# Performance work log

Measured on AMD Instinct MI355X. Metric: run time of the kernel, lower is better.

The kernel has to match this reference:

```python
import jax, jax.numpy as jnp
import numpy as np
from jax import lax

D_MODEL = 256
D_INNER = 512   # expand=2
D_STATE = 16
D_CONV = 4
DT_RANK = 16    # ceil(256/16)
HID = 128
NCLS = 4


def setup_inputs() -> dict:
    key = jax.random.key(0)
    ks = jax.random.split(key, 20)
    B, L = 4, 2048
    s = lambda *sh: 1.0 / np.sqrt(np.prod(sh[1:]) if len(sh) > 1 else sh[0])
    inp = {
        'x': jax.random.normal(ks[0], (B, L, 9), jnp.float32),
        'conv1_w': jax.random.normal(ks[1], (HID, 9, 3), jnp.float32) * s(HID, 9, 3),
        'conv1_b': jnp.zeros((HID,), jnp.float32),
        'conv2_w': jax.random.normal(ks[2], (2 * HID, HID, 3), jnp.float32) * s(2 * HID, HID, 3),
        'conv2_b': jnp.zeros((2 * HID,), jnp.float32),
        'in_proj_w': jax.random.normal(ks[3], (2 * D_INNER, D_MODEL), jnp.float32) * s(2 * D_INNER, D_MODEL),
        'dw_conv_w': jax.random.normal(ks[4], (D_INNER, 1, D_CONV), jnp.float32) * 0.5,
        'dw_conv_b': jnp.zeros((D_INNER,), jnp.float32),
        'x_proj_w': jax.random.normal(ks[5], (DT_RANK + 2 * D_STATE, D_INNER), jnp.float32) * s(1, D_INNER),
        'dt_proj_w': jax.random.normal(ks[6], (D_INNER, DT_RANK), jnp.float32) * s(D_INNER, DT_RANK),
        'dt_proj_b': jnp.log(jnp.expm1(jnp.full((D_INNER,), 0.01, jnp.float32))),  # dt init ~0.01
        'A_log': jnp.log(jnp.broadcast_to(jnp.arange(1, D_STATE + 1, dtype=jnp.float32), (D_INNER, D_STATE))).copy(),
        'D_param': jnp.ones((D_INNER,), jnp.float32),
        'out_proj_w': jax.random.normal(ks[7], (D_MODEL, D_INNER), jnp.float32) * s(D_MODEL, D_INNER),
        'fc1_w': jax.random.normal(ks[8], (HID, D_MODEL), jnp.float32) * s(HID, D_MODEL),
        'fc1_b': jnp.zeros((HID,), jnp.float32),
        'fc2_w': jax.random.normal(ks[9], (NCLS, HID), jnp.float32) * s(NCLS, HID),
        'fc2_b': jnp.zeros((NCLS,), jnp.float32),
    }
    return inp


def _conv1d(x, w, b, pad):
    # x: [B,C,L], w: [O,I,K]
    y = lax.conv_general_dilated(x, w, (1,), [pad], dimension_numbers=('NCH', 'OIH', 'NCH'))
    return y + b[None, :, None]


def _selective_scan(u, dt, Bm, Cm, A, D_param):
    # u, dt: [B,L,di]; Bm, Cm: [B,L,ds]; A: [di,ds]
    def step(h, inp):
        dt_t, b_t, c_t, u_t = inp  # [B,di],[B,ds],[B,ds],[B,di]
        dA = jnp.exp(dt_t[:, :, None] * A[None])            # [B,di,ds]
        dBu = (dt_t * u_t)[:, :, None] * b_t[:, None, :]     # [B,di,ds]
        h = dA * h + dBu
        y = jnp.einsum('bds,bs->bd', h, c_t)
        return h, y

    Bsz = u.shape[0]
    h0 = jnp.zeros((Bsz, D_INNER, D_STATE), u.dtype)
    xs = (dt.transpose(1, 0, 2), Bm.transpose(1, 0, 2), Cm.transpose(1, 0, 2), u.transpose(1, 0, 2))
    _, ys = lax.scan(step, h0, xs)
    y = ys.transpose(1, 0, 2)  # [B,L,di]
    return y + u * D_param[None, None, :]


def _forward(x, conv1_w, conv1_b, conv2_w, conv2_b, in_proj_w, dw_conv_w, dw_conv_b,
             x_proj_w, dt_proj_w, dt_proj_b, A_log, D_param, out_proj_w,
             fc1_w, fc1_b, fc2_w, fc2_b):
    # Conv feature stack
    data = x.transpose(0, 2, 1)                       # [B,9,L]
    f = jax.nn.relu(_conv1d(data, conv1_w, conv1_b, (1, 1)))
    f = jax.nn.relu(_conv1d(f, conv2_w, conv2_b, (1, 1)))
    feat = f.transpose(0, 2, 1)                       # [B,L,256]

    # Mamba block
    xz = feat @ in_proj_w.T                           # [B,L,1024]
    x_in, z = jnp.split(xz, 2, axis=-1)               # [B,L,512] each
    xc = x_in.transpose(0, 2, 1)                      # [B,512,L]
    xc = lax.conv_general_dilated(xc, dw_conv_w, (1,), [(D_CONV - 1, 0)],
                                  dimension_numbers=('NCH', 'OIH', 'NCH'),
                                  feature_group_count=D_INNER)
    xc = xc + dw_conv_b[None, :, None]
    u = jax.nn.silu(xc).transpose(0, 2, 1)            # [B,L,512]

    x_dbl = u @ x_proj_w.T                            # [B,L,48]
    dt_lr = x_dbl[..., :DT_RANK]
    Bm = x_dbl[..., DT_RANK:DT_RANK + D_STATE]
    Cm = x_dbl[..., DT_RANK + D_STATE:]
    dt = jax.nn.softplus(dt_lr @ dt_proj_w.T + dt_proj_b)  # [B,L,512]
    A = -jnp.exp(A_log)                               # [512,16]

    y = _selective_scan(u, dt, Bm, Cm, A, D_param)
    y = y * jax.nn.silu(z)
    mamba_out = y @ out_proj_w.T                      # [B,L,256]

    pooled = jnp.max(mamba_out, axis=1)               # [B,256]
    h = jax.nn.relu(pooled @ fc1_w.T + fc1_b)
    return h @ fc2_w.T + fc2_b                        # [B,4]


def reference(x, conv1_w, conv1_b, conv2_w, conv2_b, in_proj_w, dw_conv_w, dw_conv_b,
              x_proj_w, dt_proj_w, dt_proj_b, A_log, D_param, out_proj_w,
              fc1_w, fc1_b, fc2_w, fc2_b):
    return _forward(x, conv1_w, conv1_b, conv2_w, conv2_b, in_proj_w, dw_conv_w, dw_conv_b,
                    x_proj_w, dt_proj_w, dt_proj_b, A_log, D_param, out_proj_w,
                    fc1_w, fc1_b, fc2_w, fc2_b)
```

## Files before the change

### kernel.cpp

```cpp
#include <hip/hip_runtime.h>
#include <cfloat>

#define BB 4
#define LL 2048
#define DSTATE 16
#define CH 32
#define NC 64

typedef unsigned short u16;
typedef __attribute__((ext_vector_type(8))) short bf16x8;
typedef __attribute__((ext_vector_type(4))) float f32x4;

__device__ inline u16 f2b(float v) {
  union { float f; unsigned u; } c; c.f = v;
  unsigned r = c.u + 0x7fffu + ((c.u >> 16) & 1u);
  return (u16)(r >> 16);
}
__device__ inline float b2f(u16 h) {
  union { unsigned u; float f; } c; c.u = ((unsigned)h) << 16;
  return c.f;
}
__device__ inline void atomicMaxF(float* a, float v) {
  if (v >= 0.f) atomicMax((int*)a, __float_as_int(v));
  else atomicMin((unsigned int*)a, __float_as_uint(v));
}

#define GLOAD16(gsrc, ldst) \
  __builtin_amdgcn_global_load_lds( \
      (const __attribute__((address_space(1))) unsigned int*)(gsrc), \
      (__attribute__((address_space(3))) unsigned int*)(ldst), 16, 0, 0)

__global__ __launch_bounds__(256) void k1_conv1A(const float* __restrict__ x,
    const float* __restrict__ w, const float* __restrict__ bias,
    u16* __restrict__ A) {
  int idx = blockIdx.x * 256 + threadIdx.x;
  int i = idx & 127;
  int t = (idx >> 7) & (LL - 1);
  int b = idx >> 18;
  float acc = bias[i];
#pragma unroll
  for (int k = 0; k < 3; ++k) {
    int ts = t + k - 1;
    if (ts < 0 || ts >= LL) continue;
    const float* xr = x + (b * LL + ts) * 9;
    const float* wr = w + i * 27 + k;
#pragma unroll
    for (int c = 0; c < 9; ++c) acc += xr[c] * wr[c * 3];
  }
  float v = fmaxf(acc, 0.f);
  u16 h = f2b(v), l = f2b(v - b2f(h));
#pragma unroll
  for (int tap = 0; tap < 3; ++tap) {
    int rr = t + 1 - tap;
    if (rr < 0 || rr >= LL) continue;
    u16* rp = A + ((size_t)(b * LL + rr)) * 1152 + tap * 128 + i;
    rp[0] = h; rp[384] = l; rp[768] = h;
  }
  if (t == 0) {
    u16* rp = A + ((size_t)(b * LL)) * 1152 + i;
    rp[0] = 0; rp[384] = 0; rp[768] = 0;
  }
  if (t == LL - 1) {
    u16* rp = A + ((size_t)(b * LL + LL - 1)) * 1152 + 256 + i;
    rp[0] = 0; rp[384] = 0; rp[768] = 0;
  }
}

__global__ __launch_bounds__(256) void k_prep(const float* __restrict__ wc2,
    const float* __restrict__ wip, const float* __restrict__ wop,
    u16* __restrict__ dc2, u16* __restrict__ dip, u16* __restrict__ dop,
    float* __restrict__ pooled) {
  int idx = blockIdx.x * 256 + threadIdx.x;
  if (idx < 98304) {
    int o = idx / 384, r2 = idx - o * 384;
    int tap = r2 >> 7, i = r2 & 127;
    float v = wc2[o * 384 + i * 3 + tap];
    u16 h = f2b(v), l = f2b(v - b2f(h));
    u16* rp = dc2 + (size_t)o * 1152;
    rp[r2] = h; rp[384 + r2] = h; rp[768 + r2] = l;
  } else if (idx < 98304 + 262144) {
    int j = idx - 98304;
    int n = j >> 8, k = j & 255;
    float v = wip[j];
    u16 h = f2b(v), l = f2b(v - b2f(h));
    u16* rp = dip + (size_t)n * 768;
    rp[k] = h; rp[256 + k] = h; rp[512 + k] = l;
  } else if (idx < 98304 + 262144 + 131072) {
    int j = idx - 98304 - 262144;
    int n = j >> 9, k = j & 511;
    float v = wop[j];
    u16 h = f2b(v), l = f2b(v - b2f(h));
    u16* rp = dop + (size_t)n * 1536;
    rp[k] = h; rp[512 + k] = h; rp[1024 + k] = l;
  } else if (idx < 98304 + 262144 + 131072 + 1024) {
    pooled[idx - 491520] = -FLT_MAX;
  }
}

__global__ __launch_bounds__(256) void k_comb(const float* __restrict__ xw,
    const float* __restrict__ dtw, u16* __restrict__ W) {
  int idx = blockIdx.x * 256 + threadIdx.x;
  if (idx >= 576 * 512) return;
  int n = idx >> 9, k = idx & 511;
  float v = 0.f;
  if (n < 512) {
    const float* dr = dtw + n * 16;
#pragma unroll
    for (int q = 0; q < 16; ++q) v += dr[q] * xw[q * 512 + k];
  } else if (n < 544) {
    v = xw[(16 + n - 512) * 512 + k];
  }
  u16 h = f2b(v), l = f2b(v - b2f(h));
  u16* rp = W + (size_t)n * 1536;
  rp[k] = h; rp[512 + k] = h; rp[1024 + k] = l;
}

template <int TM, int TN, int EPI, int NBX>
__global__ __launch_bounds__(256) void k_mm(
    const u16* __restrict__ A, const u16* __restrict__ B,
    float* __restrict__ C, const float* __restrict__ bias,
    u16* __restrict__ osp, float* __restrict__ xdb, int N, int K) {
  constexpr int WM = TM / 2, WN = TN / 2;
  constexpr int NA = WM / 16, NB = WN / 16;
  __shared__ u16 As[2][TM * 64];
  __shared__ u16 Bs[2][TN * 64];
  __shared__ float cmw[2][TN];
  const int tid = threadIdx.x;
  const int lane = tid & 63;
  const int wid = tid >> 6;
  const int wr = wid >> 1, wc = wid & 1;
  int bid = blockIdx.y * NBX + blockIdx.x;
  int nwg = gridDim.y * NBX;
  int swz = (bid & 7) * (nwg >> 3) + (bid >> 3);
  int bm = swz / NBX;
  int bn = swz - bm * NBX;
  const int m0 = bm * TM, n0 = bn * TN;
  const int lrow = lane & 15, lg = lane >> 4;
  const int srow = tid >> 3, sg = tid & 7;
  const int NT = K >> 6;

  f32x4 acc[NA][NB] = {};

  auto stage = [&](int buf, int k0) {
#pragma unroll
    for (int r = 0; r < TM / 32; ++r) {
      int row = r * 32 + srow;
      const u16* src = A + (size_t)(m0 + row) * K + k0 + ((sg ^ (row & 7)) << 3);
      GLOAD16(src, &As[buf][row * 64 + (sg << 3)]);
    }
#pragma unroll
    for (int r = 0; r < TN / 32; ++r) {
      int row = r * 32 + srow;
      const u16* src = B + (size_t)(n0 + row) * K + k0 + ((sg ^ (row & 7)) << 3);
      GLOAD16(src, &Bs[buf][row * 64 + (sg << 3)]);
    }
  };

  stage(0, 0);
  __syncthreads();
  for (int t = 0; t < NT; ++t) {
    int cur = t & 1;
    if (t + 1 < NT) stage(cur ^ 1, (t + 1) << 6);
#pragma unroll
    for (int kc = 0; kc < 2; ++kc) {
      bf16x8 af[NA], bfr[NB];
#pragma unroll
      for (int i = 0; i < NA; ++i) {
        int row = wr * WM + i * 16 + lrow;
        int g = (kc * 4 + lg) ^ (row & 7);
        af[i] = *(const bf16x8*)&As[cur][row * 64 + (g << 3)];
      }
#pragma unroll
      for (int j = 0; j < NB; ++j) {
        int row = wc * WN + j * 16 + lrow;
        int g = (kc * 4 + lg) ^ (row & 7);
        bfr[j] = *(const bf16x8*)&Bs[cur][row * 64 + (g << 3)];
      }
#pragma unroll
      for (int i = 0; i < NA; ++i)
#pragma unroll
        for (int j = 0; j < NB; ++j)
          acc[i][j] = __builtin_amdgcn_mfma_f32_16x16x32_bf16(af[i], bfr[j], acc[i][j], 0, 0, 0);
    }
    __syncthreads();
  }
  if constexpr (EPI == 2) {
    float mj[NB];
#pragma unroll
    for (int j = 0; j < NB; ++j) {
      float m = -FLT_MAX;
#pragma unroll
      for (int i = 0; i < NA; ++i)
#pragma unroll
        for (int r = 0; r < 4; ++r) m = fmaxf(m, acc[i][j][r]);
      m = fmaxf(m, __shfl_xor(m, 16, 64));
      m = fmaxf(m, __shfl_xor(m, 32, 64));
      mj[j] = m;
    }
    if (lane < 16) {
#pragma unroll
      for (int j = 0; j < NB; ++j)
        cmw[wr][wc * WN + j * 16 + lane] = mj[j];
    }
    __syncthreads();
    if (tid < TN) {
      float v = fmaxf(cmw[0][tid], cmw[1][tid]);
      atomicMaxF(&C[(m0 >> 11) * 256 + n0 + tid], v);
    }
  } else {
#pragma unroll
    for (int i = 0; i < NA; ++i)
#pragma unroll
      for (int j = 0; j < NB; ++j)
#pragma unroll
        for (int r = 0; r < 4; ++r) {
          int row = m0 + wr * WM + i * 16 + lg * 4 + r;
          int col = n0 + wc * WN + j * 16 + lrow;
          if constexpr (EPI == 0) {
            C[(size_t)row * N + col] = acc[i][j][r];
          } else if constexpr (EPI == 1) {
            float v = fmaxf(acc[i][j][r] + bias[col], 0.f);
            u16 h = f2b(v), l = f2b(v - b2f(h));
            u16* rp = osp + (size_t)row * 768;
            rp[col] = h;
            rp[256 + col] = l;
            rp[512 + col] = h;
          } else {
            float v = acc[i][j][r];
            if (col < 512) {
              float a = v + bias[col];
              C[(size_t)row * 512 + col] = (a > 20.f) ? a : __logf(1.f + __expf(a));
            } else if (col < 544) {
              xdb[(size_t)row * 48 + 16 + (col - 512)] = v;
            }
          }
        }
  }
}

__global__ __launch_bounds__(256) void k4_dwconv(const float* __restrict__ xz,
    const float* __restrict__ w, const float* __restrict__ bias,
    u16* __restrict__ uS) {
  int idx = blockIdx.x * 256 + threadIdx.x;
  int d = idx & 511;
  int t = (idx >> 9) & (LL - 1);
  int b = idx >> 20;
  float acc = bias[d];
#pragma unroll
  for (int k = 0; k < 4; ++k) {
    int tt = t - 3 + k;
    if (tt >= 0) acc += xz[(b * LL + tt) * 1024 + d] * w[d * 4 + k];
  }
  float v = acc / (1.f + __expf(-acc));
  u16 h = f2b(v), l = f2b(v - b2f(h));
  u16* rp = uS + (size_t)(b * LL + t) * 1536 + d;
  rp[0] = h;
  rp[512] = l;
  rp[1024] = h;
}

__global__ __launch_bounds__(512) void k7a_pass1(const float* __restrict__ dt,
    const u16* __restrict__ uS, const float* __restrict__ xdbl,
    const float* __restrict__ A_log, float* __restrict__ hloc,
    float* __restrict__ dtsum) {
  __shared__ float Bs[CH][16];
  int b = blockIdx.x >> 6;
  int c = blockIdx.x & (NC - 1);
  int d = threadIdx.x;
  {
    int t = threadIdx.x >> 4, s = threadIdx.x & 15;
    Bs[t][s] = xdbl[(b * LL + c * CH + t) * 48 + 16 + s];
  }
  __syncthreads();
  float A_r[16];
#pragma unroll
  for (int s = 0; s < 16; ++s) A_r[s] = -__expf(A_log[d * 16 + s]);
  float h[16];
#pragma unroll
  for (int s = 0; s < 16; ++s) h[s] = 0.f;
  float dsum = 0.f;
  const float* dtp = dt + (size_t)(b * LL + c * CH) * 512 + d;
  const u16* up = uS + (size_t)(b * LL + c * CH) * 1536 + d;
  for (int t = 0; t < CH; ++t) {
    float dtv = dtp[t * 512];
    float uv = b2f(up[t * 1536]) + b2f(up[t * 1536 + 512]);
    float xv = dtv * uv;
    dsum += dtv;
#pragma unroll
    for (int s = 0; s < 16; ++s)
      h[s] = h[s] * __expf(dtv * A_r[s]) + xv * Bs[t][s];
  }
  int base = b * NC + c;
#pragma unroll
  for (int s = 0; s < 16; ++s) hloc[(base * 16 + s) * 512 + d] = h[s];
  dtsum[base * 512 + d] = dsum;
}

__global__ __launch_bounds__(512) void k7b_combine(const float* __restrict__ hloc,
    const float* __restrict__ dtsum, const float* __restrict__ A_log,
    float* __restrict__ h_in) {
  int g = blockIdx.x * 512 + threadIdx.x;
  int d = g & 511;
  int s = (g >> 9) & 15;
  int b = g >> 13;
  float A_r = -__expf(A_log[d * 16 + s]);
  float H = 0.f;
  for (int c = 0; c < NC; ++c) {
    int base = b * NC + c;
    h_in[(base * 16 + s) * 512 + d] = H;
    float P = __expf(A_r * dtsum[base * 512 + d]);
    H = P * H + hloc[(base * 16 + s) * 512 + d];
  }
}

__global__ __launch_bounds__(512) void k7c_pass3(const float* __restrict__ dt,
    const u16* __restrict__ uS, const float* __restrict__ xdbl,
    const float* __restrict__ xz, const float* __restrict__ A_log,
    const float* __restrict__ D_param, const float* __restrict__ h_in,
    u16* __restrict__ y2s) {
  __shared__ float BC[CH][32];
  int b = blockIdx.x >> 6;
  int c = blockIdx.x & (NC - 1);
  int d = threadIdx.x;
  for (int i = threadIdx.x; i < CH * 32; i += 512) {
    int t = i >> 5, j = i & 31;
    BC[t][j] = xdbl[(b * LL + c * CH + t) * 48 + 16 + j];
  }
  __syncthreads();
  float A_r[16];
#pragma unroll
  for (int s = 0; s < 16; ++s) A_r[s] = -__expf(A_log[d * 16 + s]);
  float Dv = D_param[d];
  int base = b * NC + c;
  float h[16];
#pragma unroll
  for (int s = 0; s < 16; ++s) h[s] = h_in[(base * 16 + s) * 512 + d];
  for (int t = 0; t < CH; ++t) {
    int row = b * LL + c * CH + t;
    float dtv = dt[(size_t)row * 512 + d];
    const u16* up = uS + (size_t)row * 1536 + d;
    float uv = b2f(up[0]) + b2f(up[512]);
    float xv = dtv * uv;
    float y = 0.f;
#pragma unroll
    for (int s = 0; s < 16; ++s) {
      h[s] = h[s] * __expf(dtv * A_r[s]) + xv * BC[t][s];
      y += h[s] * BC[t][16 + s];
    }
    float zv = xz[(size_t)row * 1024 + 512 + d];
    float sig = 1.f / (1.f + __expf(-zv));
    float v = (y + Dv * uv) * (zv * sig);
    u16 hh = f2b(v);
    u16 ll = f2b(v - b2f(hh));
    u16* rp = y2s + (size_t)row * 1536 + d;
    rp[0] = hh;
    rp[512] = ll;
    rp[1024] = hh;
  }
}

__global__ __launch_bounds__(256) void k10_head(const float* __restrict__ pooled,
    const float* __restrict__ fc1_w, const float* __restrict__ fc1_b,
    const float* __restrict__ fc2_w, const float* __restrict__ fc2_b,
    float* __restrict__ out) {
  __shared__ float pl[1024];
  __shared__ float hbuf[4][128];
  int tid = threadIdx.x;
  for (int i = tid; i < 1024; i += 256) pl[i] = pooled[i];
  __syncthreads();
  for (int idx = tid; idx < 512; idx += 256) {
    int b = idx >> 7, i = idx & 127;
    float acc = fc1_b[i];
    for (int o = 0; o < 256; ++o) acc += pl[b * 256 + o] * fc1_w[i * 256 + o];
    hbuf[b][i] = fmaxf(acc, 0.f);
  }
  __syncthreads();
  if (tid < 16) {
    int b = tid >> 2, c = tid & 3;
    float acc = fc2_b[c];
    for (int i = 0; i < 128; ++i) acc += hbuf[b][i] * fc2_w[c * 128 + i];
    out[b * 4 + c] = acc;
  }
}

extern "C" void kernel_launch(void* const* d_in, const int* in_sizes, int n_in,
                              void* d_out, int out_size, void* d_ws, size_t ws_size,
                              hipStream_t stream) {
  (void)in_sizes; (void)n_in; (void)out_size; (void)ws_size;
  const float* x        = (const float*)d_in[0];
  const float* conv1_w  = (const float*)d_in[1];
  const float* conv1_b  = (const float*)d_in[2];
  const float* conv2_w  = (const float*)d_in[3];
  const float* conv2_b  = (const float*)d_in[4];
  const float* in_proj_w= (const float*)d_in[5];
  const float* dw_w     = (const float*)d_in[6];
  const float* dw_b     = (const float*)d_in[7];
  const float* x_proj_w = (const float*)d_in[8];
  const float* dt_proj_w= (const float*)d_in[9];
  const float* dt_proj_b= (const float*)d_in[10];
  const float* A_log    = (const float*)d_in[11];
  const float* D_param  = (const float*)d_in[12];
  const float* out_proj_w=(const float*)d_in[13];
  const float* fc1_w    = (const float*)d_in[14];
  const float* fc1_b    = (const float*)d_in[15];
  const float* fc2_w    = (const float*)d_in[16];
  const float* fc2_b    = (const float*)d_in[17];
  float* out = (float*)d_out;

  float* ws    = (float*)d_ws;
  float* f1A   = ws;
  float* fe    = f1A + 4718592;
  float* wc2   = fe + 3145728;
  float* wi    = wc2 + 147456;
  float* wo    = wi + 393216;
  float* wcb   = wo + 196608;
  float* xz    = wcb + 442368;
  float* uS    = xz + 8388608;
  float* xdbl  = uS + 6291456;
  float* dt    = xdbl + 393216;
  float* y2s   = dt + 4194304;
  float* pooled= y2s + 6291456;
  float* hloc  = pooled + 1024;
  float* h_in  = hloc + 2097152;
  float* dts   = h_in + 2097152;

  u16* f1Ap = (u16*)f1A;
  u16* fep  = (u16*)fe;
  u16* wc2p = (u16*)wc2;
  u16* wip  = (u16*)wi;
  u16* wop  = (u16*)wo;
  u16* wcbp = (u16*)wcb;
  u16* uSp  = (u16*)uS;
  u16* y2p  = (u16*)y2s;

  k1_conv1A<<<dim3(BB * LL * 128 / 256), dim3(256), 0, stream>>>(x, conv1_w, conv1_b, f1Ap);
  k_prep<<<dim3(1924), dim3(256), 0, stream>>>(conv2_w, in_proj_w, out_proj_w, wc2p, wip, wop, pooled);
  k_comb<<<dim3(1152), dim3(256), 0, stream>>>(x_proj_w, dt_proj_w, wcbp);
  k_mm<32, 64, 1, 4><<<dim3(4, 256), dim3(256), 0, stream>>>(f1Ap, wc2p, nullptr, conv2_b, fep, nullptr, 256, 1152);
  k_mm<64, 64, 0, 16><<<dim3(16, 128), dim3(256), 0, stream>>>(fep, wip, xz, nullptr, nullptr, nullptr, 1024, 768);
  k4_dwconv<<<dim3(BB * LL * 512 / 256), dim3(256), 0, stream>>>(xz, dw_w, dw_b, uSp);
  k_mm<64, 64, 3, 9><<<dim3(9, 128), dim3(256), 0, stream>>>(uSp, wcbp, dt, dt_proj_b, nullptr, xdbl, 576, 1536);
  k7a_pass1<<<dim3(BB * NC), dim3(512), 0, stream>>>(dt, uSp, xdbl, A_log, hloc, dts);
  k7b_combine<<<dim3(BB * 16), dim3(512), 0, stream>>>(hloc, dts, A_log, h_in);
  k7c_pass3<<<dim3(BB * NC), dim3(512), 0, stream>>>(dt, uSp, xdbl, xz, A_log, D_param, h_in, y2p);
  k_mm<32, 64, 2, 4><<<dim3(4, 256), dim3(256), 0, stream>>>(y2p, wop, pooled, nullptr, nullptr, nullptr, 256, 1536);
  k10_head<<<dim3(1), dim3(256), 0, stream>>>(pooled, fc1_w, fc1_b, fc2_w, fc2_b, out);
}
```

Baseline: 234.7 us.

## Store split-bf16 activations as hi/lo pairs and wrap GEMM A loads

The bf16x3 split-precision GEMMs previously stored activations as three copies (hi, lo, hi) along K. They now store only hi and lo. The GEMM stage wraps its A-operand K index modulo a new KA stride, so the third segment re-reads the hi part instead of a duplicated copy. This cuts activation write traffic and footprint by a third in conv1, the conv2 epilogue, dwconv and the scan output, and scan reads use the narrower stride. The x_proj/dt_proj weight-combine kernel is also folded into k_prep, which removes one launch.

```diff
diff --git a/kernel.cpp b/kernel.cpp
--- a/kernel.cpp
+++ b/kernel.cpp
@@ -53,23 +53,24 @@
   for (int tap = 0; tap < 3; ++tap) {
     int rr = t + 1 - tap;
     if (rr < 0 || rr >= LL) continue;
-    u16* rp = A + ((size_t)(b * LL + rr)) * 1152 + tap * 128 + i;
-    rp[0] = h; rp[384] = l; rp[768] = h;
+    u16* rp = A + ((size_t)(b * LL + rr)) * 768 + tap * 128 + i;
+    rp[0] = h; rp[384] = l;
   }
   if (t == 0) {
-    u16* rp = A + ((size_t)(b * LL)) * 1152 + i;
-    rp[0] = 0; rp[384] = 0; rp[768] = 0;
+    u16* rp = A + ((size_t)(b * LL)) * 768 + i;
+    rp[0] = 0; rp[384] = 0;
   }
   if (t == LL - 1) {
-    u16* rp = A + ((size_t)(b * LL + LL - 1)) * 1152 + 256 + i;
-    rp[0] = 0; rp[384] = 0; rp[768] = 0;
+    u16* rp = A + ((size_t)(b * LL + LL - 1)) * 768 + 256 + i;
+    rp[0] = 0; rp[384] = 0;
   }
 }
 
 __global__ __launch_bounds__(256) void k_prep(const float* __restrict__ wc2,
     const float* __restrict__ wip, const float* __restrict__ wop,
+    const float* __restrict__ xw, const float* __restrict__ dtw,
     u16* __restrict__ dc2, u16* __restrict__ dip, u16* __restrict__ dop,
-    float* __restrict__ pooled) {
+    u16* __restrict__ dcb, float* __restrict__ pooled) {
   int idx = blockIdx.x * 256 + threadIdx.x;
   if (idx < 98304) {
     int o = idx / 384, r2 = idx - o * 384;
@@ -78,48 +79,44 @@
     u16 h = f2b(v), l = f2b(v - b2f(h));
     u16* rp = dc2 + (size_t)o * 1152;
     rp[r2] = h; rp[384 + r2] = h; rp[768 + r2] = l;
-  } else if (idx < 98304 + 262144) {
+  } else if (idx < 360448) {
     int j = idx - 98304;
     int n = j >> 8, k = j & 255;
     float v = wip[j];
     u16 h = f2b(v), l = f2b(v - b2f(h));
     u16* rp = dip + (size_t)n * 768;
     rp[k] = h; rp[256 + k] = h; rp[512 + k] = l;
-  } else if (idx < 98304 + 262144 + 131072) {
-    int j = idx - 98304 - 262144;
+  } else if (idx < 491520) {
+    int j = idx - 360448;
     int n = j >> 9, k = j & 511;
     float v = wop[j];
     u16 h = f2b(v), l = f2b(v - b2f(h));
     u16* rp = dop + (size_t)n * 1536;
     rp[k] = h; rp[512 + k] = h; rp[1024 + k] = l;
-  } else if (idx < 98304 + 262144 + 131072 + 1024) {
+  } else if (idx < 492544) {
     pooled[idx - 491520] = -FLT_MAX;
-  }
-}
-
-__global__ __launch_bounds__(256) void k_comb(const float* __restrict__ xw,
-    const float* __restrict__ dtw, u16* __restrict__ W) {
-  int idx = blockIdx.x * 256 + threadIdx.x;
-  if (idx >= 576 * 512) return;
-  int n = idx >> 9, k = idx & 511;
-  float v = 0.f;
-  if (n < 512) {
-    const float* dr = dtw + n * 16;
-#pragma unroll
-    for (int q = 0; q < 16; ++q) v += dr[q] * xw[q * 512 + k];
-  } else if (n < 544) {
-    v = xw[(16 + n - 512) * 512 + k];
-  }
-  u16 h = f2b(v), l = f2b(v - b2f(h));
-  u16* rp = W + (size_t)n * 1536;
-  rp[k] = h; rp[512 + k] = h; rp[1024 + k] = l;
+  } else if (idx < 787456) {
+    int j = idx - 492544;
+    int n = j >> 9, k = j & 511;
+    float v = 0.f;
+    if (n < 512) {
+      const float* dr = dtw + n * 16;
+#pragma unroll
+      for (int q = 0; q < 16; ++q) v += dr[q] * xw[q * 512 + k];
+    } else if (n < 544) {
+      v = xw[(16 + n - 512) * 512 + k];
+    }
+    u16 h = f2b(v), l = f2b(v - b2f(h));
+    u16* rp = dcb + (size_t)n * 1536;
+    rp[k] = h; rp[512 + k] = h; rp[1024 + k] = l;
+  }
 }
 
 template <int TM, int TN, int EPI, int NBX>
 __global__ __launch_bounds__(256) void k_mm(
     const u16* __restrict__ A, const u16* __restrict__ B,
     float* __restrict__ C, const float* __restrict__ bias,
-    u16* __restrict__ osp, float* __restrict__ xdb, int N, int K) {
+    u16* __restrict__ osp, float* __restrict__ xdb, int N, int K, int KA) {
   constexpr int WM = TM / 2, WN = TN / 2;
   constexpr int NA = WM / 16, NB = WN / 16;
   __shared__ u16 As[2][TM * 64];
@@ -142,10 +139,11 @@
   f32x4 acc[NA][NB] = {};
 
   auto stage = [&](int buf, int k0) {
+    int ka = (k0 < KA) ? k0 : k0 - KA;
 #pragma unroll
     for (int r = 0; r < TM / 32; ++r) {
       int row = r * 32 + srow;
-      const u16* src = A + (size_t)(m0 + row) * K + k0 + ((sg ^ (row & 7)) << 3);
+      const u16* src = A + (size_t)(m0 + row) * KA + ka + ((sg ^ (row & 7)) << 3);
       GLOAD16(src, &As[buf][row * 64 + (sg << 3)]);
     }
 #pragma unroll
@@ -221,10 +219,9 @@
           } else if constexpr (EPI == 1) {
             float v = fmaxf(acc[i][j][r] + bias[col], 0.f);
             u16 h = f2b(v), l = f2b(v - b2f(h));
-            u16* rp = osp + (size_t)row * 768;
+            u16* rp = osp + (size_t)row * 512;
             rp[col] = h;
             rp[256 + col] = l;
-            rp[512 + col] = h;
           } else {
             float v = acc[i][j][r];
             if (col < 512) {
@@ -253,10 +250,9 @@
   }
   float v = acc / (1.f + __expf(-acc));
   u16 h = f2b(v), l = f2b(v - b2f(h));
-  u16* rp = uS + (size_t)(b * LL + t) * 1536 + d;
+  u16* rp = uS + (size_t)(b * LL + t) * 1024 + d;
   rp[0] = h;
   rp[512] = l;
-  rp[1024] = h;
 }
 
 __global__ __launch_bounds__(512) void k7a_pass1(const float* __restrict__ dt,
@@ -280,10 +276,10 @@
   for (int s = 0; s < 16; ++s) h[s] = 0.f;
   float dsum = 0.f;
   const float* dtp = dt + (size_t)(b * LL + c * CH) * 512 + d;
-  const u16* up = uS + (size_t)(b * LL + c * CH) * 1536 + d;
+  const u16* up = uS + (size_t)(b * LL + c * CH) * 1024 + d;
   for (int t = 0; t < CH; ++t) {
     float dtv = dtp[t * 512];
-    float uv = b2f(up[t * 1536]) + b2f(up[t * 1536 + 512]);
+    float uv = b2f(up[t * 1024]) + b2f(up[t * 1024 + 512]);
     float xv = dtv * uv;
     dsum += dtv;
 #pragma unroll
@@ -338,7 +334,7 @@
   for (int t = 0; t < CH; ++t) {
     int row = b * LL + c * CH + t;
     float dtv = dt[(size_t)row * 512 + d];
-    const u16* up = uS + (size_t)row * 1536 + d;
+    const u16* up = uS + (size_t)row * 1024 + d;
     float uv = b2f(up[0]) + b2f(up[512]);
     float xv = dtv * uv;
     float y = 0.f;
@@ -352,10 +348,9 @@
     float v = (y + Dv * uv) * (zv * sig);
     u16 hh = f2b(v);
     u16 ll = f2b(v - b2f(hh));
-    u16* rp = y2s + (size_t)row * 1536 + d;
+    u16* rp = y2s + (size_t)row * 1024 + d;
     rp[0] = hh;
     rp[512] = ll;
-    rp[1024] = hh;
   }
 }
 
@@ -409,17 +404,17 @@
 
   float* ws    = (float*)d_ws;
   float* f1A   = ws;
-  float* fe    = f1A + 4718592;
-  float* wc2   = fe + 3145728;
+  float* fe    = f1A + 3145728;
+  float* wc2   = fe + 2097152;
   float* wi    = wc2 + 147456;
   float* wo    = wi + 393216;
   float* wcb   = wo + 196608;
   float* xz    = wcb + 442368;
   float* uS    = xz + 8388608;
-  float* xdbl  = uS + 6291456;
+  float* xdbl  = uS + 4194304;
   float* dt    = xdbl + 393216;
   float* y2s   = dt + 4194304;
-  float* pooled= y2s + 6291456;
+  float* pooled= y2s + 4194304;
   float* hloc  = pooled + 1024;
   float* h_in  = hloc + 2097152;
   float* dts   = h_in + 2097152;
@@ -434,15 +429,15 @@
   u16* y2p  = (u16*)y2s;
 
   k1_conv1A<<<dim3(BB * LL * 128 / 256), dim3(256), 0, stream>>>(x, conv1_w, conv1_b, f1Ap);
-  k_prep<<<dim3(1924), dim3(256), 0, stream>>>(conv2_w, in_proj_w, out_proj_w, wc2p, wip, wop, pooled);
-  k_comb<<<dim3(1152), dim3(256), 0, stream>>>(x_proj_w, dt_proj_w, wcbp);
-  k_mm<32, 64, 1, 4><<<dim3(4, 256), dim3(256), 0, stream>>>(f1Ap, wc2p, nullptr, conv2_b, fep, nullptr, 256, 1152);
-  k_mm<64, 64, 0, 16><<<dim3(16, 128), dim3(256), 0, stream>>>(fep, wip, xz, nullptr, nullptr, nullptr, 1024, 768);
+  k_prep<<<dim3(3076), dim3(256), 0, stream>>>(conv2_w, in_proj_w, out_proj_w,
+      x_proj_w, dt_proj_w, wc2p, wip, wop, wcbp, pooled);
+  k_mm<32, 64, 1, 4><<<dim3(4, 256), dim3(256), 0, stream>>>(f1Ap, wc2p, nullptr, conv2_b, fep, nullptr, 256, 1152, 768);
+  k_mm<64, 64, 0, 16><<<dim3(16, 128), dim3(256), 0, stream>>>(fep, wip, xz, nullptr, nullptr, nullptr, 1024, 768, 512);
   k4_dwconv<<<dim3(BB * LL * 512 / 256), dim3(256), 0, stream>>>(xz, dw_w, dw_b, uSp);
-  k_mm<64, 64, 3, 9><<<dim3(9, 128), dim3(256), 0, stream>>>(uSp, wcbp, dt, dt_proj_b, nullptr, xdbl, 576, 1536);
+  k_mm<64, 64, 3, 9><<<dim3(9, 128), dim3(256), 0, stream>>>(uSp, wcbp, dt, dt_proj_b, nullptr, xdbl, 576, 1536, 1024);
   k7a_pass1<<<dim3(BB * NC), dim3(512), 0, stream>>>(dt, uSp, xdbl, A_log, hloc, dts);
   k7b_combine<<<dim3(BB * 16), dim3(512), 0, stream>>>(hloc, dts, A_log, h_in);
   k7c_pass3<<<dim3(BB * NC), dim3(512), 0, stream>>>(dt, uSp, xdbl, xz, A_log, D_param, h_in, y2p);
-  k_mm<32, 64, 2, 4><<<dim3(4, 256), dim3(256), 0, stream>>>(y2p, wop, pooled, nullptr, nullptr, nullptr, 256, 1536);
+  k_mm<32, 64, 2, 4><<<dim3(4, 256), dim3(256), 0, stream>>>(y2p, wop, pooled, nullptr, nullptr, nullptr, 256, 1536, 1024);
   k10_head<<<dim3(1), dim3(256), 0, stream>>>(pooled, fc1_w, fc1_b, fc2_w, fc2_b, out);
 }
```

Result: no change. 230.4 us (-1.9%).
